# Kernel tuning notes

Measured on AMD Instinct MI355X. Metric: run time of the kernel, lower is better.

The kernel has to match this reference:

```python
import jax, jax.numpy as jnp
import numpy as np
import math

E = 2048         # n_embd
H = 16           # num query head pairs (num_heads)
HKV = 8          # num_kv_heads
NREP = H // HKV  # 2
HD = E // H // 2 # head_dim = 64
DEPTH = 12
LAMBDA_INIT = 0.8 - 0.6 * math.exp(-0.3 * DEPTH)
EPS = 1e-6


def setup_inputs() -> dict:
    key = jax.random.key(0)
    ks = jax.random.split(key, 10)
    s = lambda fan_in: 1.0 / np.sqrt(fan_in)
    return {
        "x": jax.random.normal(ks[0], (2, 2048, E), jnp.float32),
        "Wq": jax.random.normal(ks[1], (E, E), jnp.float32) * s(E),
        "Wk": jax.random.normal(ks[2], (E, E // NREP), jnp.float32) * s(E),
        "Wv": jax.random.normal(ks[3], (E, E // NREP), jnp.float32) * s(E),
        "Wo": jax.random.normal(ks[4], (E, E), jnp.float32) * s(E),
        "lam_q1": jax.random.normal(ks[5], (HD,), jnp.float32) * 0.1,
        "lam_k1": jax.random.normal(ks[6], (HD,), jnp.float32) * 0.1,
        "lam_q2": jax.random.normal(ks[7], (HD,), jnp.float32) * 0.1,
        "lam_k2": jax.random.normal(ks[8], (HD,), jnp.float32) * 0.1,
        "g": jnp.ones((2 * HD,), jnp.float32),  # RMSNorm weight
    }


def _rotary(x, cos, sin):
    # x: [B, T, nh, HD]; cos/sin: [T, HD//2]
    d = x.shape[-1] // 2
    x1, x2 = x[..., :d], x[..., d:]
    c = cos[None, :, None, :]
    si = sin[None, :, None, :]
    return jnp.concatenate([x1 * c + x2 * si, -x1 * si + x2 * c], axis=-1)


def reference(x, Wq, Wk, Wv, Wo, lam_q1, lam_k1, lam_q2, lam_k2, g):
    B, T, _ = x.shape
    q = (x @ Wq).reshape(B, T, 2 * H, HD)
    k = (x @ Wk).reshape(B, T, 2 * HKV, HD)
    v = (x @ Wv).reshape(B, T, HKV, 2 * HD)

    inv_freq = 1.0 / (10000.0 ** (jnp.arange(0, HD, 2, dtype=jnp.float32) / HD))
    freqs = jnp.arange(T, dtype=jnp.float32)[:, None] * inv_freq[None, :]
    cos, sin = jnp.cos(freqs), jnp.sin(freqs)
    q = _rotary(q, cos, sin)
    k = _rotary(k, cos, sin)

    q = jnp.transpose(q, (0, 2, 1, 3)) * (HD ** -0.5)   # [B, 2H, T, HD]
    k = jnp.repeat(jnp.transpose(k, (0, 2, 1, 3)), NREP, axis=1)  # [B, 2H, T, HD]
    v = jnp.repeat(jnp.transpose(v, (0, 2, 1, 3)), NREP, axis=1)  # [B, H, T, 2HD]

    scores = jnp.einsum('bhtd,bhsd->bhts', q, k)
    scores = jnp.nan_to_num(scores)
    mask = jnp.triu(jnp.full((T, T), -jnp.inf, scores.dtype), 1)
    scores = scores + mask
    p = jax.nn.softmax(scores.astype(jnp.float32), axis=-1).astype(scores.dtype)

    lam1 = jnp.exp(jnp.sum(lam_q1 * lam_k1))
    lam2 = jnp.exp(jnp.sum(lam_q2 * lam_k2))
    lam = lam1 - lam2 + LAMBDA_INIT

    p = p.reshape(B, H, 2, T, T)
    diff = p[:, :, 0] - lam * p[:, :, 1]               # [B, H, T, T]
    attn = jnp.einsum('bhts,bhsd->bhtd', diff, v)      # [B, H, T, 2HD]

    # RMSNorm over last dim (2*HD)
    attn = attn * jax.lax.rsqrt(jnp.mean(attn * attn, axis=-1, keepdims=True) + EPS) * g
    attn = attn * (1.0 - LAMBDA_INIT)
    attn = jnp.transpose(attn, (0, 2, 1, 3)).reshape(B, T, E)
    return attn @ Wo
```

## Files before the change

### kernel.cpp

```cpp
#include <hip/hip_runtime.h>

#define T_SEQ 2048

typedef __bf16 bf16x8 __attribute__((ext_vector_type(8)));
typedef float f32x4 __attribute__((ext_vector_type(4)));
typedef unsigned short u16;

__device__ __forceinline__ u16 f2b(float f) {
  unsigned u = __float_as_uint(f);
  unsigned r = 0x7fffu + ((u >> 16) & 1u);
  return (u16)((u + r) >> 16);
}
__device__ __forceinline__ float b2f(u16 v) {
  return __uint_as_float(((unsigned)v) << 16);
}
__device__ __forceinline__ f32x4 mfma16(bf16x8 a, bf16x8 b, f32x4 c) {
  return __builtin_amdgcn_mfma_f32_16x16x32_bf16(a, b, c, 0, 0, 0);
}
__device__ __forceinline__ unsigned pkhi(float lo, float hi) {
  return __builtin_amdgcn_perm(__float_as_uint(hi), __float_as_uint(lo), 0x07060302u);
}
#if defined(__has_builtin)
#if __has_builtin(__builtin_amdgcn_exp2f)
#define HAVE_RAW_EXP2 1
#endif
#endif
__device__ __forceinline__ float exp2r(float x) {
#ifdef HAVE_RAW_EXP2
  return __builtin_amdgcn_exp2f(x);
#else
  float r;
  asm("v_exp_f32 %0, %1" : "=v"(r) : "v"(x));
  return r;
#endif
}
__device__ __forceinline__ void glds16(const void* g, void* s) {
  __builtin_amdgcn_global_load_lds(
      (const __attribute__((address_space(1))) void*)(uintptr_t)g,
      (__attribute__((address_space(3))) void*)(unsigned)(uintptr_t)s, 16, 0, 0);
}

__global__ void lam_kernel(const float* __restrict__ q1, const float* __restrict__ k1,
                           const float* __restrict__ q2, const float* __restrict__ k2,
                           float* __restrict__ outp) {
  int l = threadIdx.x;
  float a = q1[l] * k1[l];
  float c = q2[l] * k2[l];
  #pragma unroll
  for (int off = 32; off > 0; off >>= 1) {
    a += __shfl_down(a, off);
    c += __shfl_down(c, off);
  }
  if (l == 0) outp[0] = expf(a) - expf(c) + 0.7836057665316244f;
}

__global__ __launch_bounds__(256) void convert_kernel(const float* __restrict__ in,
                                                      u16* __restrict__ outp, int n) {
  int i = (blockIdx.x * 256 + threadIdx.x) * 4;
  if (i >= n) return;
  float4 v = *(const float4*)(in + i);
  ushort4 pk;
  pk.x = f2b(v.x); pk.y = f2b(v.y); pk.z = f2b(v.z); pk.w = f2b(v.w);
  *(ushort4*)(outp + i) = pk;
}

__global__ __launch_bounds__(256) void transposeW_kernel(const float* __restrict__ Wq,
                                                         const float* __restrict__ Wk,
                                                         const float* __restrict__ Wv,
                                                         const float* __restrict__ Wo,
                                                         u16* __restrict__ outp) {
  __shared__ float tile[32][33];
  const int ro0 = blockIdx.y * 32;
  const int r0 = blockIdx.x * 32;
  const float* src; int C, cbase;
  if (ro0 < 2048)      { src = Wq; C = 2048; cbase = 0; }
  else if (ro0 < 3072) { src = Wk; C = 1024; cbase = 2048; }
  else if (ro0 < 4096) { src = Wv; C = 1024; cbase = 3072; }
  else                 { src = Wo; C = 2048; cbase = 4096; }
  const int cs0 = ro0 - cbase;
  const int tx = threadIdx.x & 31, ty = threadIdx.x >> 5;
  #pragma unroll
  for (int k2 = 0; k2 < 4; k2++)
    tile[ty * 4 + k2][tx] = src[(size_t)(r0 + ty * 4 + k2) * C + cs0 + tx];
  __syncthreads();
  #pragma unroll
  for (int k2 = 0; k2 < 4; k2++)
    outp[(size_t)(ro0 + ty * 4 + k2) * 2048 + r0 + tx] = f2b(tile[tx][ty * 4 + k2]);
}

#define STAGE_HALF(TILE, ROLE, BUF)                                                     \
  do {                                                                                  \
    const u16* sp_ = ((ROLE) == 0 || (ROLE) == 3 ? Ag : Bg) +                           \
                     (size_t)((ROLE) >= 2 ? 128 : 0) * K + (size_t)(TILE) * 64;         \
    u16* dp_ = ((ROLE) == 0 || (ROLE) == 3 ? &As[BUF][0] : &Bs[BUF][0]) +               \
               (((ROLE) >= 2 ? 128 : 0) + w * 8) * 64;                                  \
    glds16(sp_, dp_);                                                                   \
    glds16(sp_ + (size_t)64 * K, dp_ + 4096);                                           \
  } while (0)

#define PHASE(I, J, BUF, NEWA, NEWB, BN, STILE, SROLE, SBUF, DOVM)                      \
  do {                                                                                  \
    if (NEWA) {                                                                         \
      _Pragma("unroll") for (int u_ = 0; u_ < 4; u_++) {                                \
        const int ar_ = ((I) * 4 + u_) * 32 + wm * 16 + l15;                            \
        _Pragma("unroll") for (int kk_ = 0; kk_ < 2; kk_++)                             \
            am[u_][kk_] = *(const bf16x8*)&As[BUF][ar_ * 64 +                           \
                              (((kk_ * 4 + quad) ^ (ar_ & 7)) << 3)];                   \
      }                                                                                 \
    }                                                                                   \
    if (NEWB) {                                                                         \
      _Pragma("unroll") for (int v_ = 0; v_ < 2; v_++) {                                \
        const int br_ = ((J) * 2 + v_) * 64 + wn * 16 + l15;                            \
        _Pragma("unroll") for (int kk_ = 0; kk_ < 2; kk_++)                             \
            BN[v_][kk_] = *(const bf16x8*)&Bs[BUF][br_ * 64 +                           \
                              (((kk_ * 4 + quad) ^ (br_ & 7)) << 3)];                   \
      }                                                                                 \
    }                                                                                   \
    STAGE_HALF(STILE, SROLE, SBUF);                                                     \
    __builtin_amdgcn_s_barrier();                                                       \
    asm volatile("s_waitcnt lgkmcnt(0)" ::: "memory");                                  \
    __builtin_amdgcn_sched_barrier(0);                                                  \
    __builtin_amdgcn_s_setprio(1);                                                      \
    _Pragma("unroll") for (int u_ = 0; u_ < 4; u_++)                                    \
        _Pragma("unroll") for (int v_ = 0; v_ < 2; v_++) {                              \
      acc[(I) * 4 + u_][(J) * 2 + v_] =                                                 \
          mfma16(am[u_][0], BN[v_][0], acc[(I) * 4 + u_][(J) * 2 + v_]);                \
      acc[(I) * 4 + u_][(J) * 2 + v_] =                                                 \
          mfma16(am[u_][1], BN[v_][1], acc[(I) * 4 + u_][(J) * 2 + v_]);                \
    }                                                                                   \
    __builtin_amdgcn_s_setprio(0);                                                      \
    if (DOVM) asm volatile("s_waitcnt vmcnt(6)" ::: "memory");                          \
    __builtin_amdgcn_s_barrier();                                                       \
  } while (0)

__global__ __launch_bounds__(512, 2) void gemm256_kernel(const u16* __restrict__ A,
                                                         const u16* __restrict__ BT,
                                                         u16* __restrict__ C, int N, int K) {
  __shared__ alignas(16) u16 As[2][256 * 64];
  __shared__ alignas(16) u16 Bs[2][256 * 64];
  const int tid = threadIdx.x, w = tid >> 6, lane = tid & 63;
  const int l15 = lane & 15, quad = lane >> 4;
  const int wm = w >> 2, wn = w & 3;
  const int lr = lane >> 3, slot = lane & 7, csw = slot ^ lr;
  const int m0 = blockIdx.y * 256, n0 = blockIdx.x * 256;
  const int nkt = K >> 6;

  f32x4 acc[8][4];
  #pragma unroll
  for (int r = 0; r < 8; r++)
    #pragma unroll
    for (int s = 0; s < 4; s++) acc[r][s] = (f32x4){0.f, 0.f, 0.f, 0.f};

  const u16* Ag = A + (size_t)(m0 + w * 8 + lr) * K + csw * 8;
  const u16* Bg = BT + (size_t)(n0 + w * 8 + lr) * K + csw * 8;

  bf16x8 am[4][2], bn0[2][2], bn1[2][2];

  STAGE_HALF(0, 0, 0); STAGE_HALF(0, 1, 0); STAGE_HALF(0, 2, 0); STAGE_HALF(0, 3, 0);
  STAGE_HALF(1, 0, 1); STAGE_HALF(1, 1, 1); STAGE_HALF(1, 2, 1);
  asm volatile("s_waitcnt vmcnt(6)" ::: "memory");
  __builtin_amdgcn_s_barrier();

  #pragma unroll 1
  for (int t = 0; t < nkt; t += 2) {
    PHASE(0, 0, 0, 1, 1, bn0, t + 1, 3, 1, 0);
    PHASE(0, 1, 0, 0, 1, bn1, t + 2, 0, 0, 0);
    PHASE(1, 0, 0, 1, 0, bn0, t + 2, 1, 0, 0);
    PHASE(1, 1, 0, 0, 0, bn1, t + 2, 2, 0, 1);
    PHASE(0, 0, 1, 1, 1, bn0, t + 2, 3, 0, 0);
    PHASE(0, 1, 1, 0, 1, bn1, t + 3, 0, 1, 0);
    PHASE(1, 0, 1, 1, 0, bn0, t + 3, 1, 1, 0);
    PHASE(1, 1, 1, 0, 0, bn1, t + 3, 2, 1, 1);
  }

  const int crow = m0 + wm * 16 + quad * 4;
  const int ccol = n0 + wn * 16 + l15;
  #pragma unroll
  for (int r = 0; r < 8; r++)
    #pragma unroll
    for (int s = 0; s < 4; s++)
      #pragma unroll
      for (int rr = 0; rr < 4; rr++)
        C[(size_t)(crow + r * 32 + rr) * N + ccol + s * 64] = f2b(acc[r][s][rr]);
}

#define OSTAGE(TILE, CH, BUF)                                                           \
  do {                                                                                  \
    if ((CH) == 0) {                                                                    \
      glds16(Ag + (size_t)(TILE) * 64, &As[BUF][0] + w * 512);                          \
      glds16(Ag + (size_t)64 * K + (size_t)(TILE) * 64, &As[BUF][4096] + w * 512);      \
      glds16(Bg + (size_t)(TILE) * 64, &Bs[BUF][0] + w * 512);                          \
    } else {                                                                            \
      glds16(Bg + (size_t)64 * K + (size_t)(TILE) * 64, &Bs[BUF][4096] + w * 512);      \
      glds16(Bg + (size_t)128 * K + (size_t)(TILE) * 64, &Bs[BUF][8192] + w * 512);     \
      glds16(Bg + (size_t)192 * K + (size_t)(TILE) * 64, &Bs[BUF][12288] + w * 512);    \
    }                                                                                   \
  } while (0)

#define OPHASE(BUF, J, NEWA, STILE, SCH, SBUF, DOVM)                                    \
  do {                                                                                  \
    if (NEWA) {                                                                         \
      _Pragma("unroll") for (int fr_ = 0; fr_ < 4; fr_++) {                             \
        const int ar_ = wm * 64 + fr_ * 16 + l15;                                       \
        _Pragma("unroll") for (int kk_ = 0; kk_ < 2; kk_++)                             \
            am[fr_][kk_] = *(const bf16x8*)&As[BUF][ar_ * 64 +                          \
                               (((kk_ * 4 + quad) ^ (ar_ & 7)) << 3)];                  \
      }                                                                                 \
    }                                                                                   \
    _Pragma("unroll") for (int v_ = 0; v_ < 2; v_++) {                                  \
      const int br_ = ((J) * 2 + v_) * 64 + wn * 16 + l15;                              \
      _Pragma("unroll") for (int kk_ = 0; kk_ < 2; kk_++)                               \
          bn[v_][kk_] = *(const bf16x8*)&Bs[BUF][br_ * 64 +                             \
                            (((kk_ * 4 + quad) ^ (br_ & 7)) << 3)];                     \
    }                                                                                   \
    OSTAGE(STILE, SCH, SBUF);                                                           \
    __builtin_amdgcn_s_barrier();                                                       \
    asm volatile("s_waitcnt lgkmcnt(0)" ::: "memory");                                  \
    __builtin_amdgcn_sched_barrier(0);                                                  \
    __builtin_amdgcn_s_setprio(1);                                                      \
    _Pragma("unroll") for (int fr_ = 0; fr_ < 4; fr_++)                                 \
        _Pragma("unroll") for (int v_ = 0; v_ < 2; v_++) {                              \
      acc[fr_][(J) * 2 + v_] = mfma16(am[fr_][0], bn[v_][0], acc[fr_][(J) * 2 + v_]);   \
      acc[fr_][(J) * 2 + v_] = mfma16(am[fr_][1], bn[v_][1], acc[fr_][(J) * 2 + v_]);   \
    }                                                                                   \
    __builtin_amdgcn_s_setprio(0);                                                      \
    if (DOVM) asm volatile("s_waitcnt vmcnt(3)" ::: "memory");                          \
    __builtin_amdgcn_s_barrier();                                                       \
  } while (0)

__global__ __launch_bounds__(512, 2) void gemm128x256_kernel(const u16* __restrict__ A,
                                                             const u16* __restrict__ BT,
                                                             float* __restrict__ C,
                                                             int N, int K) {
  __shared__ alignas(16) u16 As[2][128 * 64];
  __shared__ alignas(16) u16 Bs[2][256 * 64];
  const int tid = threadIdx.x, w = tid >> 6, lane = tid & 63;
  const int l15 = lane & 15, quad = lane >> 4;
  const int wm = w >> 2, wn = w & 3;
  const int lr = lane >> 3, slot = lane & 7, csw = slot ^ lr;
  const int m0 = blockIdx.y * 128, n0 = blockIdx.x * 256;
  const int nkt = K >> 6;

  f32x4 acc[4][4];
  #pragma unroll
  for (int r = 0; r < 4; r++)
    #pragma unroll
    for (int s = 0; s < 4; s++) acc[r][s] = (f32x4){0.f, 0.f, 0.f, 0.f};

  const u16* Ag = A + (size_t)(m0 + w * 8 + lr) * K + csw * 8;
  const u16* Bg = BT + (size_t)(n0 + w * 8 + lr) * K + csw * 8;

  bf16x8 am[4][2], bn[2][2];

  OSTAGE(0, 0, 0); OSTAGE(0, 1, 0); OSTAGE(1, 0, 1);
  asm volatile("s_waitcnt vmcnt(3)" ::: "memory");
  __builtin_amdgcn_s_barrier();

  #pragma unroll 1
  for (int t = 0; t < nkt; t += 2) {
    OPHASE(0, 0, 1, t + 1, 1, 1, 0);
    OPHASE(0, 1, 0, t + 2, 0, 0, 1);
    OPHASE(1, 0, 1, t + 2, 1, 0, 0);
    OPHASE(1, 1, 0, t + 3, 0, 1, 1);
  }

  const int crow = m0 + wm * 64 + quad * 4;
  #pragma unroll
  for (int r = 0; r < 4; r++)
    #pragma unroll
    for (int s = 0; s < 4; s++) {
      const int col = n0 + s * 64 + wn * 16 + l15;
      #pragma unroll
      for (int rr = 0; rr < 4; rr++)
        C[(size_t)(crow + r * 16 + rr) * N + col] = acc[r][s][rr];
    }
}

__global__ __launch_bounds__(256) void rotab_kernel(float* __restrict__ ct,
                                                    float* __restrict__ st) {
  int idx = blockIdx.x * 256 + threadIdx.x;
  int i = idx & 31, t = idx >> 5;
  float invf = exp2f(-(float)i * 0.4152410118609203f);
  float ang = (float)t * invf;
  ct[idx] = cosf(ang);
  st[idx] = sinf(ang);
}

__global__ __launch_bounds__(256) void rotary_kernel(const u16* __restrict__ qkv,
                                                     const float* __restrict__ ct,
                                                     const float* __restrict__ st,
                                                     u16* __restrict__ Qb,
                                                     u16* __restrict__ Kb, float qscale) {
  int idx = blockIdx.x * 256 + threadIdx.x;
  int i4 = (idx & 7) * 4;
  int bt = (idx >> 3) & 4095;
  int hh = idx >> 15;
  int t = bt & (T_SEQ - 1), b = bt >> 11;
  bool isq = hh < 32;
  int col = isq ? hh * 64 : 2048 + (hh - 32) * 64;
  size_t inb = (size_t)bt * 4096 + col + i4;
  ushort4 xa = *(const ushort4*)(qkv + inb);
  ushort4 xb = *(const ushort4*)(qkv + inb + 32);
  float4 c4 = *(const float4*)(ct + t * 32 + i4);
  float4 s4 = *(const float4*)(st + t * 32 + i4);
  float scale = isq ? qscale : 1.0f;
  ushort4 o1, o2;
  {
    float x1 = b2f(xa.x), x2 = b2f(xb.x);
    o1.x = f2b((x1 * c4.x + x2 * s4.x) * scale);
    o2.x = f2b((x2 * c4.x - x1 * s4.x) * scale);
  }
  {
    float x1 = b2f(xa.y), x2 = b2f(xb.y);
    o1.y = f2b((x1 * c4.y + x2 * s4.y) * scale);
    o2.y = f2b((x2 * c4.y - x1 * s4.y) * scale);
  }
  {
    float x1 = b2f(xa.z), x2 = b2f(xb.z);
    o1.z = f2b((x1 * c4.z + x2 * s4.z) * scale);
    o2.z = f2b((x2 * c4.z - x1 * s4.z) * scale);
  }
  {
    float x1 = b2f(xa.w), x2 = b2f(xb.w);
    o1.w = f2b((x1 * c4.w + x2 * s4.w) * scale);
    o2.w = f2b((x2 * c4.w - x1 * s4.w) * scale);
  }
  u16* outp = isq ? (Qb + (size_t)(b * 32 + hh) * (T_SEQ * 64))
                  : (Kb + (size_t)(b * 16 + hh - 32) * (T_SEQ * 64));
  size_t ob = (size_t)t * 64 + i4;
  *(ushort4*)(outp + ob) = o1;
  *(ushort4*)(outp + ob + 32) = o2;
}

__global__ __launch_bounds__(256) void vtrans_kernel(const u16* __restrict__ qkv,
                                                     u16* __restrict__ outp) {
  __shared__ unsigned tile[32][33];
  int bh = blockIdx.z;
  int t0 = blockIdx.x * 32, dv0 = blockIdx.y * 32;
  int tx = threadIdx.x & 31, ty = threadIdx.x >> 5;
  int bt_base = (bh >> 3) * T_SEQ;
  int col = 3072 + (bh & 7) * 128 + dv0 + tx;
  #pragma unroll
  for (int k2 = 0; k2 < 4; k2++)
    tile[ty * 4 + k2][tx] = qkv[(size_t)(bt_base + t0 + ty * 4 + k2) * 4096 + col];
  __syncthreads();
  const int stile = t0 >> 6;
  const int sold = (t0 & 63) + tx;
  const int slo = sold & 31, hb = sold >> 5;
  const int sp = hb * 32 + ((slo >> 2) & 3) * 8 + ((slo >> 4) & 1) * 4 + (slo & 3);
  #pragma unroll
  for (int k2 = 0; k2 < 4; k2++) {
    int dv = dv0 + ty * 4 + k2;
    outp[(((size_t)bh * 32 + stile) * 128 + dv) * 64 + sp] = (u16)tile[tx][ty * 4 + k2];
  }
}

__global__ __launch_bounds__(256) void attn_kernel(const u16* __restrict__ Qb,
                                                   const u16* __restrict__ Kb,
                                                   const u16* __restrict__ Vt,
                                                   const float* __restrict__ lamp,
                                                   const float* __restrict__ g,
                                                   u16* __restrict__ attn_out) {
  __shared__ alignas(16) char smem[49152];
  u16* const Ks0 = (u16*)smem;
  u16* const Vs0 = (u16*)(smem + 16384);
  u16* const Psb = (u16*)smem;
  const int pr = blockIdx.x;
  const int bh = blockIdx.y;
  const int b = bh >> 4, h = bh & 15;
  const int tid = threadIdx.x, w = tid >> 6, lane = tid & 63;
  const int l15 = lane & 15, quad = lane >> 4;
  const int lr = lane >> 3, slot = lane & 7, csw = slot ^ lr;
  const float lam = lamp[0];

  const u16* Kg = Kb + (size_t)(b * 16 + h) * (T_SEQ * 64) + (w * 16 + lr) * 64 + csw * 8;
  const u16* Vg = Vt + (size_t)(b * 8 + (h >> 1)) * (T_SEQ * 128) + w * 2048 + lr * 64 + csw * 8;
  u16* kd[2] = {Ks0 + w * 1024, Ks0 + 4096 + w * 1024};
  u16* vd[2] = {Vs0 + w * 2048, Vs0 + 8192 + w * 2048};

  #pragma unroll 1
  for (int half = 0; half < 2; half++) {
    const int tt = half ? 31 - pr : pr;
    const int qb = tt * 64 + w * 16;
    const int qglob = qb + l15;

    bf16x8 qf[2][2];
    #pragma unroll
    for (int e = 0; e < 2; e++)
      #pragma unroll
      for (int kk = 0; kk < 2; kk++)
        qf[e][kk] = *(const bf16x8*)&Qb[((size_t)(b * 32 + 2 * h + e) * T_SEQ + qb + l15) * 64 +
                                        kk * 32 + quad * 8];

    f32x4 o[2][8];
    float lsum[2] = {0.f, 0.f};
    #pragma unroll
    for (int e = 0; e < 2; e++)
      #pragma unroll
      for (int nt = 0; nt < 8; nt++) o[e][nt] = (f32x4){0.f, 0.f, 0.f, 0.f};

    {
      glds16(Kg, kd[0]); glds16(Kg + 512, kd[0] + 512);
      glds16(Vg, vd[0]); glds16(Vg + 512, vd[0] + 512);
      glds16(Vg + 1024, vd[0] + 1024); glds16(Vg + 1536, vd[0] + 1536);
    }
    __syncthreads();

    #pragma unroll 1
    for (int st = 0; st <= tt; st++) {
      const int buf = st & 1;
      const u16* Ksb = Ks0 + buf * 4096;
      const u16* Vsb = Vs0 + buf * 8192;
      if (st < tt) {
        const u16* kp = Kg + (size_t)(st + 1) * 4096;
        const u16* vp = Vg + (size_t)(st + 1) * 8192;
        glds16(kp, kd[buf ^ 1]); glds16(kp + 512, kd[buf ^ 1] + 512);
        glds16(vp, vd[buf ^ 1]); glds16(vp + 512, vd[buf ^ 1] + 512);
        glds16(vp + 1024, vd[buf ^ 1] + 1024); glds16(vp + 1536, vd[buf ^ 1] + 1536);
      }

      bf16x8 kf[4][2];
      #pragma unroll
      for (int j = 0; j < 4; j++) {
        const int rk = j * 16 + l15;
        #pragma unroll
        for (int kk = 0; kk < 2; kk++)
          kf[j][kk] = *(const bf16x8*)&Ksb[rk * 64 + (((kk * 4 + quad) ^ (rk & 7)) << 3)];
      }

      bf16x8 pa[2][2];
      #pragma unroll
      for (int e = 0; e < 2; e++) {
        f32x4 sc[4];
        __builtin_amdgcn_s_setprio(1);
        #pragma unroll
        for (int j = 0; j < 4; j++) {
          f32x4 z = {0.f, 0.f, 0.f, 0.f};
          z = mfma16(kf[j][0], qf[e][0], z);
          sc[j] = mfma16(kf[j][1], qf[e][1], z);
        }
        __builtin_amdgcn_s_setprio(0);
        if (st == tt) {
          #pragma unroll
          for (int j = 0; j < 4; j++) {
            int srow = st * 64 + j * 16 + quad * 4;
            #pragma unroll
            for (int rr = 0; rr < 4; rr++)
              if (srow + rr > qglob) sc[j][rr] = -1e30f;
          }
        }
        float ls = 0.f;
        union { unsigned u[8]; bf16x8 v[2]; } pk;
        #pragma unroll
        for (int j = 0; j < 4; j++) {
          #pragma unroll
          for (int rr = 0; rr < 4; rr++) {
            float p = exp2r(sc[j][rr]);
            sc[j][rr] = p;
            ls += p;
          }
          pk.u[j * 2] = pkhi(sc[j][0], sc[j][1]);
          pk.u[j * 2 + 1] = pkhi(sc[j][2], sc[j][3]);
        }
        pa[e][0] = pk.v[0];
        pa[e][1] = pk.v[1];
        lsum[e] += ls;
      }
      __builtin_amdgcn_s_setprio(1);
      #pragma unroll
      for (int nt = 0; nt < 8; nt++) {
        const int rv = nt * 16 + l15;
        bf16x8 vf0 = *(const bf16x8*)&Vsb[rv * 64 + ((quad ^ (rv & 7)) << 3)];
        bf16x8 vf1 = *(const bf16x8*)&Vsb[rv * 64 + (((4 + quad) ^ (rv & 7)) << 3)];
        o[0][nt] = mfma16(vf0, pa[0][0], o[0][nt]);
        o[0][nt] = mfma16(vf1, pa[0][1], o[0][nt]);
        o[1][nt] = mfma16(vf0, pa[1][0], o[1][nt]);
        o[1][nt] = mfma16(vf1, pa[1][1], o[1][nt]);
      }
      __builtin_amdgcn_s_setprio(0);
      __syncthreads();
    }

    float l0 = lsum[0], l1 = lsum[1];
    l0 += __shfl_xor(l0, 16); l0 += __shfl_xor(l0, 32);
    l1 += __shfl_xor(l1, 16); l1 += __shfl_xor(l1, 32);
    const float il0 = 1.f / l0, il1 = lam / l1;
    float ssq = 0.f;
    #pragma unroll
    for (int nt = 0; nt < 8; nt++)
      #pragma unroll
      for (int rr = 0; rr < 4; rr++) {
        float v = o[0][nt][rr] * il0 - o[1][nt][rr] * il1;
        o[0][nt][rr] = v;
        ssq += v * v;
      }
    ssq += __shfl_xor(ssq, 16);
    ssq += __shfl_xor(ssq, 32);
    const float rsc = rsqrtf(ssq * (1.f / 128.f) + 1e-6f) * 0.2163942334683756f;
    #pragma unroll
    for (int nt = 0; nt < 8; nt++) {
      float4 gv = *(const float4*)&g[nt * 16 + quad * 4];
      uint2 pk;
      pk.x = (unsigned)f2b(o[0][nt][0] * rsc * gv.x) |
             ((unsigned)f2b(o[0][nt][1] * rsc * gv.y) << 16);
      pk.y = (unsigned)f2b(o[0][nt][2] * rsc * gv.z) |
             ((unsigned)f2b(o[0][nt][3] * rsc * gv.w) << 16);
      *(uint2*)&Psb[(w * 16 + l15) * 136 + nt * 16 + quad * 4] = pk;
    }
    asm volatile("s_waitcnt lgkmcnt(0)" ::: "memory");
    __builtin_amdgcn_sched_barrier(0);
    #pragma unroll
    for (int i = 0; i < 4; i++) {
      const int r = (lane >> 4) + i * 4, c = (lane & 15) * 8;
      bf16x8 ov = *(const bf16x8*)&Psb[(w * 16 + r) * 136 + c];
      *(bf16x8*)&attn_out[(size_t)(b * T_SEQ + qb + r) * 2048 + h * 128 + c] = ov;
    }
    __syncthreads();
  }
}

extern "C" void kernel_launch(void* const* d_in, const int* in_sizes, int n_in, void* d_out,
                              int out_size, void* d_ws, size_t ws_size, hipStream_t stream) {
  const float* x = (const float*)d_in[0];
  const float* Wq = (const float*)d_in[1];
  const float* Wk = (const float*)d_in[2];
  const float* Wv = (const float*)d_in[3];
  const float* Wo = (const float*)d_in[4];
  const float* lq1 = (const float*)d_in[5];
  const float* lk1 = (const float*)d_in[6];
  const float* lq2 = (const float*)d_in[7];
  const float* lk2 = (const float*)d_in[8];
  const float* g = (const float*)d_in[9];

  char* ws = (char*)d_ws;
  u16* WT = (u16*)(ws);
  u16* xbf = (u16*)(ws + 25165824);
  u16* QKV = (u16*)(ws + 41943040);
  u16* Qb = (u16*)(ws + 75497472);
  u16* Kb = (u16*)(ws + 92274688);
  u16* Vt = (u16*)(ws + 100663296);
  u16* Attn = (u16*)(ws + 109051904);
  float* lam = (float*)(ws + 125829120);
  float* ct = (float*)(ws + 25165824);
  float* st = (float*)(ws + 25165824 + 262144);

  lam_kernel<<<1, 64, 0, stream>>>(lq1, lk1, lq2, lk2, lam);
  convert_kernel<<<8192, 256, 0, stream>>>(x, xbf, 8388608);
  transposeW_kernel<<<dim3(64, 192), 256, 0, stream>>>(Wq, Wk, Wv, Wo, WT);
  gemm256_kernel<<<dim3(16, 16), 512, 0, stream>>>(xbf, WT, QKV, 4096, 2048);
  rotab_kernel<<<256, 256, 0, stream>>>(ct, st);
  rotary_kernel<<<6144, 256, 0, stream>>>(QKV, ct, st, Qb, Kb, 0.18033688011112042f);
  vtrans_kernel<<<dim3(64, 4, 16), 256, 0, stream>>>(QKV, Vt);
  attn_kernel<<<dim3(16, 32), 256, 0, stream>>>(Qb, Kb, Vt, lam, g, Attn);
  gemm128x256_kernel<<<dim3(8, 32), 512, 0, stream>>>(Attn, WT + (size_t)4096 * 2048,
                                                      (float*)d_out, 2048, 2048);
}
```

Baseline: 320.2 us.

## Restructure attention into 512-thread blocks over 128-row query tiles

```diff
diff --git a/kernel.cpp b/kernel.cpp
--- a/kernel.cpp
+++ b/kernel.cpp
@@ -355,167 +355,166 @@
   }
 }
 
-__global__ __launch_bounds__(256) void attn_kernel(const u16* __restrict__ Qb,
-                                                   const u16* __restrict__ Kb,
-                                                   const u16* __restrict__ Vt,
-                                                   const float* __restrict__ lamp,
-                                                   const float* __restrict__ g,
-                                                   u16* __restrict__ attn_out) {
+__global__ __launch_bounds__(512, 2) void attn_kernel(const u16* __restrict__ Qb,
+                                                      const u16* __restrict__ Kb,
+                                                      const u16* __restrict__ Vt,
+                                                      const float* __restrict__ lamp,
+                                                      const float* __restrict__ g,
+                                                      u16* __restrict__ attn_out) {
   __shared__ alignas(16) char smem[49152];
   u16* const Ks0 = (u16*)smem;
   u16* const Vs0 = (u16*)(smem + 16384);
   u16* const Psb = (u16*)smem;
-  const int pr = blockIdx.x;
-  const int bh = blockIdx.y;
+  const int id = blockIdx.x;
+  const int araw = id & 15;
+  const int bh = (id >> 4) & 31;
+  const int a = (id < 256) ? 15 - araw : araw;
   const int b = bh >> 4, h = bh & 15;
   const int tid = threadIdx.x, w = tid >> 6, lane = tid & 63;
   const int l15 = lane & 15, quad = lane >> 4;
   const int lr = lane >> 3, slot = lane & 7, csw = slot ^ lr;
   const float lam = lamp[0];
 
-  const u16* Kg = Kb + (size_t)(b * 16 + h) * (T_SEQ * 64) + (w * 16 + lr) * 64 + csw * 8;
-  const u16* Vg = Vt + (size_t)(b * 8 + (h >> 1)) * (T_SEQ * 128) + w * 2048 + lr * 64 + csw * 8;
-  u16* kd[2] = {Ks0 + w * 1024, Ks0 + 4096 + w * 1024};
-  u16* vd[2] = {Vs0 + w * 2048, Vs0 + 8192 + w * 2048};
+  const int tlast = 2 * a + 1;
+  const int myTile = 2 * a + (w >> 2);
+  const int qb = a * 128 + w * 16;
+  const int qglob = qb + l15;
+
+  const u16* Kg = Kb + (size_t)(b * 16 + h) * (T_SEQ * 64) + (w * 8 + lr) * 64 + csw * 8;
+  const u16* Vg = Vt + (size_t)(b * 8 + (h >> 1)) * (T_SEQ * 128) + w * 1024 + lr * 64 + csw * 8;
+  u16* kd[2] = {Ks0 + w * 512, Ks0 + 4096 + w * 512};
+  u16* vd[2] = {Vs0 + w * 1024, Vs0 + 8192 + w * 1024};
+
+  bf16x8 qf[2][2];
+  #pragma unroll
+  for (int e = 0; e < 2; e++)
+    #pragma unroll
+    for (int kk = 0; kk < 2; kk++)
+      qf[e][kk] = *(const bf16x8*)&Qb[((size_t)(b * 32 + 2 * h + e) * T_SEQ + qb + l15) * 64 +
+                                      kk * 32 + quad * 8];
+
+  f32x4 o[2][8];
+  float lsum[2] = {0.f, 0.f};
+  #pragma unroll
+  for (int e = 0; e < 2; e++)
+    #pragma unroll
+    for (int nt = 0; nt < 8; nt++) o[e][nt] = (f32x4){0.f, 0.f, 0.f, 0.f};
+
+  glds16(Kg, kd[0]);
+  glds16(Vg, vd[0]); glds16(Vg + 512, vd[0] + 512);
 
   #pragma unroll 1
-  for (int half = 0; half < 2; half++) {
-    const int tt = half ? 31 - pr : pr;
-    const int qb = tt * 64 + w * 16;
-    const int qglob = qb + l15;
-
-    bf16x8 qf[2][2];
-    #pragma unroll
-    for (int e = 0; e < 2; e++)
+  for (int st = 0; st <= tlast; st++) {
+    const int buf = st & 1;
+    const u16* Ksb = Ks0 + buf * 4096;
+    const u16* Vsb = Vs0 + buf * 8192;
+    if (st < tlast) {
+      const u16* kp = Kg + (size_t)(st + 1) * 4096;
+      const u16* vp = Vg + (size_t)(st + 1) * 8192;
+      glds16(kp, kd[buf ^ 1]);
+      glds16(vp, vd[buf ^ 1]); glds16(vp + 512, vd[buf ^ 1] + 512);
+      asm volatile("s_waitcnt vmcnt(3)" ::: "memory");
+    } else {
+      asm volatile("s_waitcnt vmcnt(0)" ::: "memory");
+    }
+    __builtin_amdgcn_s_barrier();
+    __builtin_amdgcn_sched_barrier(0);
+
+    bf16x8 kf[4][2];
+    #pragma unroll
+    for (int j = 0; j < 4; j++) {
+      const int rk = j * 16 + l15;
       #pragma unroll
       for (int kk = 0; kk < 2; kk++)
-        qf[e][kk] = *(const bf16x8*)&Qb[((size_t)(b * 32 + 2 * h + e) * T_SEQ + qb + l15) * 64 +
-                                        kk * 32 + quad * 8];
-
-    f32x4 o[2][8];
-    float lsum[2] = {0.f, 0.f};
-    #pragma unroll
-    for (int e = 0; e < 2; e++)
-      #pragma unroll
-      for (int nt = 0; nt < 8; nt++) o[e][nt] = (f32x4){0.f, 0.f, 0.f, 0.f};
-
-    {
-      glds16(Kg, kd[0]); glds16(Kg + 512, kd[0] + 512);
-      glds16(Vg, vd[0]); glds16(Vg + 512, vd[0] + 512);
-      glds16(Vg + 1024, vd[0] + 1024); glds16(Vg + 1536, vd[0] + 1536);
+        kf[j][kk] = *(const bf16x8*)&Ksb[rk * 64 + (((kk * 4 + quad) ^ (rk & 7)) << 3)];
     }
-    __syncthreads();
-
-    #pragma unroll 1
-    for (int st = 0; st <= tt; st++) {
-      const int buf = st & 1;
-      const u16* Ksb = Ks0 + buf * 4096;
-      const u16* Vsb = Vs0 + buf * 8192;
-      if (st < tt) {
-        const u16* kp = Kg + (size_t)(st + 1) * 4096;
-        const u16* vp = Vg + (size_t)(st + 1) * 8192;
-        glds16(kp, kd[buf ^ 1]); glds16(kp + 512, kd[buf ^ 1] + 512);
-        glds16(vp, vd[buf ^ 1]); glds16(vp + 512, vd[buf ^ 1] + 512);
-        glds16(vp + 1024, vd[buf ^ 1] + 1024); glds16(vp + 1536, vd[buf ^ 1] + 1536);
-      }
-
-      bf16x8 kf[4][2];
+
+    bf16x8 pa[2][2];
+    #pragma unroll
+    for (int e = 0; e < 2; e++) {
+      f32x4 sc[4];
+      __builtin_amdgcn_s_setprio(1);
       #pragma unroll
       for (int j = 0; j < 4; j++) {
-        const int rk = j * 16 + l15;
-        #pragma unroll
-        for (int kk = 0; kk < 2; kk++)
-          kf[j][kk] = *(const bf16x8*)&Ksb[rk * 64 + (((kk * 4 + quad) ^ (rk & 7)) << 3)];
+        f32x4 z = {0.f, 0.f, 0.f, 0.f};
+        z = mfma16(kf[j][0], qf[e][0], z);
+        sc[j] = mfma16(kf[j][1], qf[e][1], z);
       }
-
-      bf16x8 pa[2][2];
-      #pragma unroll
-      for (int e = 0; e < 2; e++) {
-        f32x4 sc[4];
-        __builtin_amdgcn_s_setprio(1);
+      __builtin_amdgcn_s_setprio(0);
+      if (st >= myTile) {
         #pragma unroll
         for (int j = 0; j < 4; j++) {
-          f32x4 z = {0.f, 0.f, 0.f, 0.f};
-          z = mfma16(kf[j][0], qf[e][0], z);
-          sc[j] = mfma16(kf[j][1], qf[e][1], z);
+          int srow = st * 64 + j * 16 + quad * 4;
+          #pragma unroll
+          for (int rr = 0; rr < 4; rr++)
+            if (srow + rr > qglob) sc[j][rr] = -1e30f;
         }
-        __builtin_amdgcn_s_setprio(0);
-        if (st == tt) {
-          #pragma unroll
-          for (int j = 0; j < 4; j++) {
-            int srow = st * 64 + j * 16 + quad * 4;
-            #pragma unroll
-            for (int rr = 0; rr < 4; rr++)
-              if (srow + rr > qglob) sc[j][rr] = -1e30f;
-          }
+      }
+      float ls = 0.f;
+      union { unsigned u[8]; bf16x8 v[2]; } pk;
+      #pragma unroll
+      for (int j = 0; j < 4; j++) {
+        #pragma unroll
+        for (int rr = 0; rr < 4; rr++) {
+          float p = exp2r(sc[j][rr]);
+          sc[j][rr] = p;
+          ls += p;
         }
-        float ls = 0.f;
-        union { unsigned u[8]; bf16x8 v[2]; } pk;
-        #pragma unroll
-        for (int j = 0; j < 4; j++) {
-          #pragma unroll
-          for (int rr = 0; rr < 4; rr++) {
-            float p = exp2r(sc[j][rr]);
-            sc[j][rr] = p;
-            ls += p;
-          }
-          pk.u[j * 2] = pkhi(sc[j][0], sc[j][1]);
-          pk.u[j * 2 + 1] = pkhi(sc[j][2], sc[j][3]);
-        }
-        pa[e][0] = pk.v[0];
-        pa[e][1] = pk.v[1];
-        lsum[e] += ls;
+        pk.u[j * 2] = pkhi(sc[j][0], sc[j][1]);
+        pk.u[j * 2 + 1] = pkhi(sc[j][2], sc[j][3]);
       }
-      __builtin_amdgcn_s_setprio(1);
-      #pragma unroll
-      for (int nt = 0; nt < 8; nt++) {
-        const int rv = nt * 16 + l15;
-        bf16x8 vf0 = *(const bf16x8*)&Vsb[rv * 64 + ((quad ^ (rv & 7)) << 3)];
-        bf16x8 vf1 = *(const bf16x8*)&Vsb[rv * 64 + (((4 + quad) ^ (rv & 7)) << 3)];
-        o[0][nt] = mfma16(vf0, pa[0][0], o[0][nt]);
-        o[0][nt] = mfma16(vf1, pa[0][1], o[0][nt]);
-        o[1][nt] = mfma16(vf0, pa[1][0], o[1][nt]);
-        o[1][nt] = mfma16(vf1, pa[1][1], o[1][nt]);
-      }
-      __builtin_amdgcn_s_setprio(0);
-      __syncthreads();
+      pa[e][0] = pk.v[0];
+      pa[e][1] = pk.v[1];
+      lsum[e] += ls;
     }
-
-    float l0 = lsum[0], l1 = lsum[1];
-    l0 += __shfl_xor(l0, 16); l0 += __shfl_xor(l0, 32);
-    l1 += __shfl_xor(l1, 16); l1 += __shfl_xor(l1, 32);
-    const float il0 = 1.f / l0, il1 = lam / l1;
-    float ssq = 0.f;
-    #pragma unroll
-    for (int nt = 0; nt < 8; nt++)
-      #pragma unroll
-      for (int rr = 0; rr < 4; rr++) {
-        float v = o[0][nt][rr] * il0 - o[1][nt][rr] * il1;
-        o[0][nt][rr] = v;
-        ssq += v * v;
-      }
-    ssq += __shfl_xor(ssq, 16);
-    ssq += __shfl_xor(ssq, 32);
-    const float rsc = rsqrtf(ssq * (1.f / 128.f) + 1e-6f) * 0.2163942334683756f;
+    __builtin_amdgcn_s_setprio(1);
     #pragma unroll
     for (int nt = 0; nt < 8; nt++) {
-      float4 gv = *(const float4*)&g[nt * 16 + quad * 4];
-      uint2 pk;
-      pk.x = (unsigned)f2b(o[0][nt][0] * rsc * gv.x) |
-             ((unsigned)f2b(o[0][nt][1] * rsc * gv.y) << 16);
-      pk.y = (unsigned)f2b(o[0][nt][2] * rsc * gv.z) |
-             ((unsigned)f2b(o[0][nt][3] * rsc * gv.w) << 16);
-      *(uint2*)&Psb[(w * 16 + l15) * 136 + nt * 16 + quad * 4] = pk;
+      const int rv = nt * 16 + l15;
+      bf16x8 vf0 = *(const bf16x8*)&Vsb[rv * 64 + ((quad ^ (rv & 7)) << 3)];
+      bf16x8 vf1 = *(const bf16x8*)&Vsb[rv * 64 + (((4 + quad) ^ (rv & 7)) << 3)];
+      o[0][nt] = mfma16(vf0, pa[0][0], o[0][nt]);
+      o[0][nt] = mfma16(vf1, pa[0][1], o[0][nt]);
+      o[1][nt] = mfma16(vf0, pa[1][0], o[1][nt]);
+      o[1][nt] = mfma16(vf1, pa[1][1], o[1][nt]);
     }
-    asm volatile("s_waitcnt lgkmcnt(0)" ::: "memory");
-    __builtin_amdgcn_sched_barrier(0);
-    #pragma unroll
-    for (int i = 0; i < 4; i++) {
-      const int r = (lane >> 4) + i * 4, c = (lane & 15) * 8;
-      bf16x8 ov = *(const bf16x8*)&Psb[(w * 16 + r) * 136 + c];
-      *(bf16x8*)&attn_out[(size_t)(b * T_SEQ + qb + r) * 2048 + h * 128 + c] = ov;
+    __builtin_amdgcn_s_setprio(0);
+    __builtin_amdgcn_s_barrier();
+  }
+
+  float l0 = lsum[0], l1 = lsum[1];
+  l0 += __shfl_xor(l0, 16); l0 += __shfl_xor(l0, 32);
+  l1 += __shfl_xor(l1, 16); l1 += __shfl_xor(l1, 32);
+  const float il0 = 1.f / l0, il1 = lam / l1;
+  float ssq = 0.f;
+  #pragma unroll
+  for (int nt = 0; nt < 8; nt++)
+    #pragma unroll
+    for (int rr = 0; rr < 4; rr++) {
+      float v = o[0][nt][rr] * il0 - o[1][nt][rr] * il1;
+      o[0][nt][rr] = v;
+      ssq += v * v;
     }
-    __syncthreads();
+  ssq += __shfl_xor(ssq, 16);
+  ssq += __shfl_xor(ssq, 32);
+  const float rsc = rsqrtf(ssq * (1.f / 128.f) + 1e-6f) * 0.2163942334683756f;
+  #pragma unroll
+  for (int nt = 0; nt < 8; nt++) {
+    float4 gv = *(const float4*)&g[nt * 16 + quad * 4];
+    uint2 pk;
+    pk.x = (unsigned)f2b(o[0][nt][0] * rsc * gv.x) |
+           ((unsigned)f2b(o[0][nt][1] * rsc * gv.y) << 16);
+    pk.y = (unsigned)f2b(o[0][nt][2] * rsc * gv.z) |
+           ((unsigned)f2b(o[0][nt][3] * rsc * gv.w) << 16);
+    *(uint2*)&Psb[(w * 16 + l15) * 136 + nt * 16 + quad * 4] = pk;
+  }
+  asm volatile("s_waitcnt lgkmcnt(0)" ::: "memory");
+  __builtin_amdgcn_sched_barrier(0);
+  #pragma unroll
+  for (int i = 0; i < 4; i++) {
+    const int r = (lane >> 4) + i * 4, c = (lane & 15) * 8;
+    bf16x8 ov = *(const bf16x8*)&Psb[(w * 16 + r) * 136 + c];
+    *(bf16x8*)&attn_out[(size_t)(b * T_SEQ + qb + r) * 2048 + h * 128 + c] = ov;
   }
 }
 
@@ -551,7 +550,7 @@
   rotab_kernel<<<256, 256, 0, stream>>>(ct, st);
   rotary_kernel<<<6144, 256, 0, stream>>>(QKV, ct, st, Qb, Kb, 0.18033688011112042f);
   vtrans_kernel<<<dim3(64, 4, 16), 256, 0, stream>>>(QKV, Vt);
-  attn_kernel<<<dim3(16, 32), 256, 0, stream>>>(Qb, Kb, Vt, lam, g, Attn);
+  attn_kernel<<<512, 512, 0, stream>>>(Qb, Kb, Vt, lam, g, Attn);
   gemm128x256_kernel<<<dim3(8, 32), 512, 0, stream>>>(Attn, WT + (size_t)4096 * 2048,
                                                       (float*)d_out, 2048, 2048);
 }
```

New measurement: 333.5 us. 4.1% more time.
